# Performance work log

Hardware: AMD Instinct MI355X
Metric: run time of the kernel (lower is better)

Reference implementation:

```python
import jax, jax.numpy as jnp
import numpy as np


def _icosa_group():
    """60 rotation matrices of the icosahedral rotation group (vertex anchors)."""
    phi = (1.0 + 5.0 ** 0.5) / 2.0

    def rot(axis, ang):
        a = np.asarray(axis, dtype=np.float64)
        a = a / np.linalg.norm(a)
        K = np.array([[0.0, -a[2], a[1]], [a[2], 0.0, -a[0]], [-a[1], a[0], 0.0]])
        return np.eye(3) + np.sin(ang) * K + (1.0 - np.cos(ang)) * (K @ K)

    # two distinct 5-fold vertex axes generate the full group of order 60
    gens = [rot([0.0, 1.0, phi], 2.0 * np.pi / 5.0),
            rot([0.0, -1.0, phi], 2.0 * np.pi / 5.0)]
    mats = {tuple(np.round(np.eye(3), 6).ravel()): np.eye(3)}
    frontier = [np.eye(3)]
    while frontier:
        new = []
        for m in frontier:
            for g in gens:
                p = g @ m
                k = tuple(np.round(p, 6).ravel())
                if k not in mats:
                    mats[k] = p
                    new.append(p)
        frontier = new
    Rs = np.stack([mats[k] for k in sorted(mats.keys())]).astype(np.float32)
    assert Rs.shape[0] == 60
    return Rs


def _normalize(x, axis=-1, eps=1e-12):
    n = jnp.linalg.norm(x, axis=axis, keepdims=True)
    return x / jnp.maximum(n, eps)


def setup_inputs() -> dict:
    key = jax.random.key(0)
    ks = jax.random.split(key, 6)
    bs, P, N = 2, 1024, 16
    d_in, d_out, K = 64, 32, 7
    neighbor_index = jax.random.randint(ks[0], (bs, P, N), 0, P, dtype=jnp.int32)
    vertices = jax.random.normal(ks[1], (bs, P, 3), dtype=jnp.float32)
    feature_map = jax.random.normal(ks[2], (bs, d_in, P, 3), dtype=jnp.float32)
    W = jax.random.normal(ks[3], (d_out, d_in, K, 3), dtype=jnp.float32) * (2.0 / (d_in * K * 3 + d_out * K * 3)) ** 0.5
    W_center = jax.random.normal(ks[4], (d_out, d_in), dtype=jnp.float32) * (2.0 / (d_in + d_out)) ** 0.5
    directions = jax.random.normal(ks[5], (d_out, K, 3), dtype=jnp.float32) * (2.0 / (d_out * 3 + K * 3)) ** 0.5
    Rs = jnp.asarray(_icosa_group())
    return {"neighbor_index": neighbor_index, "vertices": vertices,
            "feature_map": feature_map, "W": W, "W_center": W_center,
            "directions": directions, "Rs": Rs}


def reference(neighbor_index, vertices, feature_map, W, W_center, directions, Rs):
    bs, P, N = neighbor_index.shape
    d_out, d_in, K, _ = W.shape
    n_bin = 5
    interval = Rs.shape[0] // n_bin

    # neighbor direction unit vectors [b,p,n,3]
    nbrs = jax.vmap(lambda v_b, i_b: v_b[i_b])(vertices, neighbor_index)
    ndn = _normalize(nbrs - vertices[:, :, None, :])
    kd = _normalize(directions)  # [d,k,3]

    # ---- stage 1: rotation search (fully detached in the torch original) ----
    ndn_s = jax.lax.stop_gradient(ndn)
    kd_s = jax.lax.stop_gradient(kd)
    W_s = jax.lax.stop_gradient(W)
    fm_s = jax.lax.stop_gradient(feature_map)
    Rs_s = jax.lax.stop_gradient(Rs)

    r_vals, r_idxs = [], []
    for i in range(n_bin):
        Rsi = Rs_s[i * interval:(i + 1) * interval]  # [r,3,3]
        kd_ro = jnp.einsum('dkj,rij->dkir', kd_s, Rsi)          # [d,k,3,r]
        theta = jnp.einsum('dkjr,bpnj->bdkpnr', kd_ro, ndn_s)   # [b,d,k,p,n,r]
        W_ro = jnp.einsum('dckj,rij->dckir', W_s, Rsi)          # [d,c,k,3,r]
        fo = jnp.einsum('dckir,bcpi->bdkpr', W_ro, fm_s)        # [b,d,k,p,r]
        gathered = jax.vmap(lambda f_b, i_b: f_b[:, :, i_b, :])(fo, neighbor_index)  # [b,d,k,p,n,r]
        ka = gathered * theta
        ka = jnp.max(ka, axis=4)   # max over neighbors -> [b,d,k,p,r]
        ka = jnp.sum(ka, axis=2)   # sum over kernel pts -> [b,d,p,r]
        r_vals.append(jnp.max(ka, axis=-1))
        r_idxs.append(jnp.argmax(ka, axis=-1) + i * interval)
    r_vals = jnp.stack(r_vals, axis=-1)  # [b,d,p,5]
    r_idxs = jnp.stack(r_idxs, axis=-1)  # [b,d,p,5]
    best_bin = jnp.argmax(r_vals, axis=-1)  # [b,d,p]
    r_index = jnp.take_along_axis(r_idxs, best_bin[..., None], axis=-1)[..., 0]  # [b,d,p]
    match_R = Rs[r_index]  # [b,d,p,3,3]

    # ---- stage 2: apply best rotation (differentiable) ----
    kd_ro2 = jnp.einsum('dkj,bdpij->bdkpi', kd, match_R)               # [b,d,k,p,3]
    theta2 = jax.nn.relu(jnp.einsum('bdkpj,bpnj->bdkpn', kd_ro2, ndn))  # [b,d,k,p,n]
    fo2 = jnp.einsum('dckj,bdpij,bcpi->bdkp', W, match_R, feature_map)  # [b,d,k,p]
    gathered2 = jax.vmap(lambda f_b, i_b: f_b[:, :, i_b])(fo2, neighbor_index)  # [b,d,k,p,n]
    ka2 = gathered2 * theta2
    kaw2 = jnp.max(ka2, axis=4)  # [b,d,k,p]
    out = jnp.einsum('bdkp,bdkpi->bdpi', kaw2, kd_ro2)
    center = jnp.einsum('dc,bcpi->bdpi', W_center, feature_map)
    return out + center
```

## Files before the change

### kernel.cpp

```cpp
#include <hip/hip_runtime.h>
#include <math.h>

#define BS   2
#define PP   1024
#define NN   16
#define CIN  64
#define DOUT 32
#define KK   7
#define NR   60
#define NT2  30

#define OFF_NDN  0
#define OFF_KROT 98304
#define OFF_M    138624
#define OFF_PVAL 4332928
#define OFF_PIDX 6299008
#define OFF_FO2  6790528
#define OFF_RIDX 7314816

#define NEG_INF (-3.402823466e38f)

typedef float v2f __attribute__((ext_vector_type(2)));
typedef float v4f __attribute__((ext_vector_type(4)));

__device__ __forceinline__ float sload(const float* __restrict__ p, int idx) {
    return __int_as_float(__builtin_amdgcn_readfirstlane(__float_as_int(p[idx])));
}

__device__ __forceinline__ v2f pk_mul_sv(v2f s, v2f v) {
    v2f d; asm("v_pk_mul_f32 %0, %1, %2" : "=v"(d) : "s"(s), "v"(v)); return d;
}
__device__ __forceinline__ v2f pk_fma_svv(v2f s, v2f v, v2f c) {
    v2f d; asm("v_pk_fma_f32 %0, %1, %2, %3" : "=v"(d) : "s"(s), "v"(v), "v"(c)); return d;
}
__device__ __forceinline__ v2f pk_mul_vv(v2f a, v2f b) {
    v2f d; asm("v_pk_mul_f32 %0, %1, %2" : "=v"(d) : "v"(a), "v"(b)); return d;
}

__device__ __forceinline__ float quad_max(float x) {
    float y = __int_as_float(__builtin_amdgcn_mov_dpp(
        __float_as_int(x), 0xB1, 0xF, 0xF, true));
    x = fmaxf(x, y);
    float z = __int_as_float(__builtin_amdgcn_mov_dpp(
        __float_as_int(x), 0x4E, 0xF, 0xF, true));
    return fmaxf(x, z);
}

__global__ __launch_bounds__(256) void k_pre(const int* __restrict__ nbr,
                                             const float* __restrict__ vert,
                                             const float* __restrict__ dirs,
                                             const float* __restrict__ Rs,
                                             float* __restrict__ ws) {
    int tid = blockIdx.x * 256 + threadIdx.x;
    if (tid < BS * PP * NN) {
        int p = (tid >> 4) & (PP - 1);
        int b = tid >> 14;
        int q = nbr[tid];
        const float* vp = vert + ((b << 10) + p) * 3;
        const float* vq = vert + ((b << 10) + q) * 3;
        float dx = vq[0] - vp[0], dy = vq[1] - vp[1], dz = vq[2] - vp[2];
        float nrm = sqrtf(dx * dx + dy * dy + dz * dz);
        float den = fmaxf(nrm, 1e-12f);
        dx /= den; dy /= den; dz /= den;
        float* o = ws + OFF_NDN + tid * 3;
        o[0] = dx; o[1] = dy; o[2] = dz;
    }
    int t2 = tid - BS * PP * NN;
    if (t2 >= 0 && t2 < DOUT * NR * KK) {
        int k = t2 % KK;
        int r = (t2 / KK) % NR;
        int d = t2 / (KK * NR);
        const float* dk = dirs + (d * KK + k) * 3;
        float x = dk[0], y = dk[1], z = dk[2];
        float nrm = sqrtf(x * x + y * y + z * z);
        float den = fmaxf(nrm, 1e-12f);
        x /= den; y /= den; z /= den;
        const float* R = Rs + r * 9;
        float* o = ws + OFF_KROT + t2 * 3;
        o[0] = R[0] * x + R[1] * y + R[2] * z;
        o[1] = R[3] * x + R[4] * y + R[5] * z;
        o[2] = R[6] * x + R[7] * y + R[8] * z;
    }
}

__global__ __launch_bounds__(256, 2) void k_buildM(const float* __restrict__ fm,
                                                   const float* __restrict__ W,
                                                   float* __restrict__ Mout) {
    int d = blockIdx.y, b = blockIdx.z;
    int p = blockIdx.x * 256 + threadIdx.x;

    float M[64];
#pragma unroll
    for (int t = 0; t < 64; t++) M[t] = 0.f;

    const float* fbase = fm + (size_t)(b * CIN * PP + p) * 3;
    const float* wbase = W + (size_t)d * CIN * KK * 3;
    for (int c = 0; c < CIN; c++) {
        const float* f = fbase + c * PP * 3;
        float f0 = f[0], f1 = f[1], f2 = f[2];
        const float* wl = wbase + c * 21;
#pragma unroll
        for (int k = 0; k < KK; k++) {
#pragma unroll
            for (int j = 0; j < 3; j++) {
                float w = sload(wl, k * 3 + j);
                M[k * 9 + 0 + j] += w * f0;
                M[k * 9 + 3 + j] += w * f1;
                M[k * 9 + 6 + j] += w * f2;
            }
        }
    }
    float4* o = (float4*)(Mout + (size_t)(((b * DOUT + d) << 10) + p) * 64);
#pragma unroll
    for (int t = 0; t < 15; t++)
        o[t] = make_float4(M[4 * t], M[4 * t + 1], M[4 * t + 2], M[4 * t + 3]);
    o[15] = make_float4(M[60], M[61], M[62], 0.f);
}

__device__ __forceinline__ int fo_base(int p) {
    return (p << 2) ^ ((p >> 1) & 7);
}

__global__ __launch_bounds__(1024)
void k_score(const int* __restrict__ nbr,
             const float* __restrict__ Rs,
             const float* __restrict__ Mptr,
             const float* __restrict__ ndn,
             const float* __restrict__ krot,
             float* __restrict__ pval,
             unsigned char* __restrict__ pidx8) {
    __shared__ v4f fo4s[PP * 4];
    const int tile = blockIdx.x, d = blockIdx.y, b = blockIdx.z;
    const int bd = b * DOUT + d;
    const int rbase = tile * 2;
    const int tq = threadIdx.x >> 2;
    const int ns = threadIdx.x & 3;

    {
        const int p = threadIdx.x;
        float Rc0[9], Rc1[9];
#pragma unroll
        for (int j = 0; j < 9; j++) {
            Rc0[j] = sload(Rs, (rbase + 0) * 9 + j);
            Rc1[j] = sload(Rs, (rbase + 1) * 9 + j);
        }
        float fo0[KK], fo1[KK];
#pragma unroll
        for (int k = 0; k < KK; k++) { fo0[k] = 0.f; fo1[k] = 0.f; }

        const float4* m4 = (const float4*)(Mptr + (size_t)((bd << 10) + p) * 64);
#pragma unroll
        for (int t = 0; t < 16; t++) {
            float4 v = m4[t];
            float e[4] = {v.x, v.y, v.z, v.w};
#pragma unroll
            for (int ee = 0; ee < 4; ee++) {
                const int g = 4 * t + ee;
                if (g < 63) {
                    const int k = g / 9, r9 = g % 9;
                    fo0[k] += Rc0[r9] * e[ee];
                    fo1[k] += Rc1[r9] * e[ee];
                }
            }
            if ((t & 3) == 3)
                __builtin_amdgcn_sched_barrier(0);
        }
        const int fb = fo_base(p);
        v4f s0; s0.x = fo0[0]; s0.y = fo1[0]; s0.z = fo0[1]; s0.w = fo1[1];
        v4f s1; s1.x = fo0[2]; s1.y = fo1[2]; s1.z = fo0[3]; s1.w = fo1[3];
        v4f s2; s2.x = fo0[4]; s2.y = fo1[4]; s2.z = fo0[5]; s2.w = fo1[5];
        v4f s3; s3.x = fo0[6]; s3.y = fo1[6]; s3.z = 0.f;    s3.w = 0.f;
        fo4s[fb]     = s0;
        fo4s[fb ^ 1] = s1;
        fo4s[fb ^ 2] = s2;
        fo4s[fb ^ 3] = s3;
    }
    __syncthreads();

    v2f vkp[KK][3];
    {
        const int kb0 = (d * NR + rbase + 0) * 21;
        const int kb1 = (d * NR + rbase + 1) * 21;
#pragma unroll
        for (int k = 0; k < KK; k++)
#pragma unroll
            for (int c = 0; c < 3; c++) {
                v2f t; t.x = sload(krot, kb0 + k * 3 + c);
                       t.y = sload(krot, kb1 + k * 3 + c);
                vkp[k][c] = t;
            }
    }
    const v2f* fo2s = (const v2f*)fo4s;

#pragma unroll
    for (int pp = 0; pp < 4; pp++) {
        const int p2 = (pp << 8) + tq;

        int4 nv = *(const int4*)(nbr + (((size_t)((b << 10) + p2)) << 4) + (ns << 2));
        float u[12];
        {
            const float4* u4 = (const float4*)(ndn + ((size_t)((b << 10) + p2) * 16 + (ns << 2)) * 3);
            float4 a = u4[0], bb = u4[1], cc = u4[2];
            u[0] = a.x;  u[1] = a.y;  u[2] = a.z;  u[3] = a.w;
            u[4] = bb.x; u[5] = bb.y; u[6] = bb.z; u[7] = bb.w;
            u[8] = cc.x; u[9] = cc.y; u[10] = cc.z; u[11] = cc.w;
        }

        float mk0[KK], mk1[KK];
#pragma unroll
        for (int k = 0; k < KK; k++) { mk0[k] = NEG_INF; mk1[k] = NEG_INF; }

        int c0 = fo_base(nv.x);
        v4f A = fo4s[c0];
        v4f B = fo4s[c0 ^ 1];
        v4f C = fo4s[c0 ^ 2];
        v2f D = fo2s[(c0 ^ 3) << 1];

#pragma unroll
        for (int n = 0; n < 4; n++) {
            v4f An, Bn, Cn; v2f Dn;
            if (n < 3) {
                int qn = (n == 0) ? nv.y : (n == 1) ? nv.z : nv.w;
                int cn = fo_base(qn);
                An = fo4s[cn];
                Bn = fo4s[cn ^ 1];
                Cn = fo4s[cn ^ 2];
                Dn = fo2s[(cn ^ 3) << 1];
            }
            float u0 = u[n * 3], u1 = u[n * 3 + 1], u2 = u[n * 3 + 2];
            v2f u00; u00.x = u0; u00.y = u0;
            v2f u11; u11.x = u1; u11.y = u1;
            v2f u22; u22.x = u2; u22.y = u2;
#pragma unroll
            for (int k = 0; k < KK; k++) {
                v2f g;
                if (k == 0)      g = __builtin_shufflevector(A, A, 0, 1);
                else if (k == 1) g = __builtin_shufflevector(A, A, 2, 3);
                else if (k == 2) g = __builtin_shufflevector(B, B, 0, 1);
                else if (k == 3) g = __builtin_shufflevector(B, B, 2, 3);
                else if (k == 4) g = __builtin_shufflevector(C, C, 0, 1);
                else if (k == 5) g = __builtin_shufflevector(C, C, 2, 3);
                else             g = D;
                v2f t = pk_mul_sv(vkp[k][0], u00);
                t = pk_fma_svv(vkp[k][1], u11, t);
                t = pk_fma_svv(vkp[k][2], u22, t);
                v2f pr = pk_mul_vv(g, t);
                mk0[k] = fmaxf(mk0[k], pr.x);
                mk1[k] = fmaxf(mk1[k], pr.y);
            }
            if (n < 3) { A = An; B = Bn; C = Cn; D = Dn; }
            __builtin_amdgcn_sched_barrier(0);
        }
#pragma unroll
        for (int k = 0; k < KK; k++) {
            mk0[k] = quad_max(mk0[k]);
            mk1[k] = quad_max(mk1[k]);
        }
        float s0 = ((mk0[0] + mk0[1]) + (mk0[2] + mk0[3])) + ((mk0[4] + mk0[5]) + mk0[6]);
        float s1 = ((mk1[0] + mk1[1]) + (mk1[2] + mk1[3])) + ((mk1[4] + mk1[5]) + mk1[6]);
        float bl = s0; int bil = rbase;
        if (s1 > bl) { bl = s1; bil = rbase + 1; }

        if (ns == 0) {
            int pi = (bd * NT2 + tile) * PP + p2;
            pval[pi] = bl;
            pidx8[pi] = (unsigned char)bil;
        }
    }
}

__global__ __launch_bounds__(256, 2) void k_reduce(const float* __restrict__ Rs,
                                                   float* __restrict__ ws) {
    int gid = blockIdx.x * 256 + threadIdx.x;
    int bd = gid >> 10;
    int p = gid & (PP - 1);
    const unsigned char* pidx8 = (const unsigned char*)(ws + OFF_PIDX);
    float best = NEG_INF;
    int bi = 0;
    for (int t = 0; t < NT2; t++) {
        float v = ws[OFF_PVAL + (bd * NT2 + t) * PP + p];
        int idx = pidx8[(bd * NT2 + t) * PP + p];
        if (v > best) { best = v; bi = idx; }
    }
    ((int*)ws)[OFF_RIDX + gid] = bi;

    const float* R = Rs + bi * 9;
    float R0 = R[0], R1 = R[1], R2 = R[2];
    float R3 = R[3], R4 = R[4], R5 = R[5];
    float R6 = R[6], R7 = R[7], R8 = R[8];

    float M[64];
    const float4* m4 = (const float4*)(ws + OFF_M + (size_t)gid * 64);
#pragma unroll
    for (int t = 0; t < 16; t++) {
        float4 v = m4[t];
        M[4 * t] = v.x; M[4 * t + 1] = v.y; M[4 * t + 2] = v.z; M[4 * t + 3] = v.w;
    }
    float* o = ws + OFF_FO2 + (size_t)gid * 8;
#pragma unroll
    for (int k = 0; k < KK; k++) {
        o[k] = R0 * M[k * 9 + 0] + R1 * M[k * 9 + 1] + R2 * M[k * 9 + 2]
             + R3 * M[k * 9 + 3] + R4 * M[k * 9 + 4] + R5 * M[k * 9 + 5]
             + R6 * M[k * 9 + 6] + R7 * M[k * 9 + 7] + R8 * M[k * 9 + 8];
    }
    o[7] = 0.f;
}

__global__ __launch_bounds__(256, 2) void k_final(const int* __restrict__ nbr,
                                                  const float* __restrict__ fm,
                                                  const float* __restrict__ Wc,
                                                  const float* __restrict__ ws,
                                                  float* __restrict__ out) {
    __shared__ float fo2_s[PP * 8];
    __shared__ float krot_s[NR * KK * 3];
    int d = blockIdx.y, b = blockIdx.z;
    int bd = b * DOUT + d;
    for (int i = threadIdx.x; i < PP * 8; i += 256)
        fo2_s[i] = ws[OFF_FO2 + (size_t)bd * PP * 8 + i];
    for (int i = threadIdx.x; i < NR * KK * 3; i += 256)
        krot_s[i] = ws[OFF_KROT + d * NR * KK * 3 + i];
    __syncthreads();

    int p = blockIdx.x * 256 + threadIdx.x;
    int gid = (bd << 10) + p;
    int ri = ((const int*)ws)[OFF_RIDX + gid];

    float v[21];
#pragma unroll
    for (int t = 0; t < 21; t++) v[t] = krot_s[ri * 21 + t];

    float u[48];
    {
        const float4* u4 = (const float4*)(ws + OFF_NDN + (size_t)((b << 10) + p) * 48);
#pragma unroll
        for (int t = 0; t < 12; t++) {
            float4 w = u4[t];
            u[4 * t] = w.x; u[4 * t + 1] = w.y; u[4 * t + 2] = w.z; u[4 * t + 3] = w.w;
        }
    }
    int nidx[16];
    {
        const int4* n4 = (const int4*)(nbr + (size_t)((b << 10) + p) * 16);
#pragma unroll
        for (int t = 0; t < 4; t++) {
            int4 w = n4[t];
            nidx[4 * t] = w.x; nidx[4 * t + 1] = w.y; nidx[4 * t + 2] = w.z; nidx[4 * t + 3] = w.w;
        }
    }

    float kaw[7];
#pragma unroll
    for (int k = 0; k < KK; k++) kaw[k] = NEG_INF;
#pragma unroll
    for (int n = 0; n < NN; n++) {
        int q = nidx[n];
        const float4* fq = (const float4*)&fo2_s[q * 8];
        float4 a = fq[0], c4 = fq[1];
        float g[7] = {a.x, a.y, a.z, a.w, c4.x, c4.y, c4.z};
        float u0 = u[n * 3], u1 = u[n * 3 + 1], u2 = u[n * 3 + 2];
#pragma unroll
        for (int k = 0; k < KK; k++) {
            float th = fmaxf(v[k * 3] * u0 + v[k * 3 + 1] * u1 + v[k * 3 + 2] * u2, 0.f);
            kaw[k] = fmaxf(kaw[k], g[k] * th);
        }
    }
    float o0 = 0.f, o1 = 0.f, o2 = 0.f;
#pragma unroll
    for (int k = 0; k < KK; k++) {
        o0 += kaw[k] * v[k * 3];
        o1 += kaw[k] * v[k * 3 + 1];
        o2 += kaw[k] * v[k * 3 + 2];
    }
    const float* fbase = fm + (size_t)(b * CIN * PP + p) * 3;
    const float* wrow = Wc + d * CIN;
    for (int c = 0; c < CIN; c++) {
        float wcv = sload(wrow, c);
        const float* f = fbase + c * PP * 3;
        o0 += wcv * f[0];
        o1 += wcv * f[1];
        o2 += wcv * f[2];
    }
    out[(size_t)gid * 3 + 0] = o0;
    out[(size_t)gid * 3 + 1] = o1;
    out[(size_t)gid * 3 + 2] = o2;
}

extern "C" void kernel_launch(void* const* d_in, const int* in_sizes, int n_in,
                              void* d_out, int out_size, void* d_ws, size_t ws_size,
                              hipStream_t stream) {
    const int*   nbr  = (const int*)d_in[0];
    const float* vert = (const float*)d_in[1];
    const float* fm   = (const float*)d_in[2];
    const float* W    = (const float*)d_in[3];
    const float* Wc   = (const float*)d_in[4];
    const float* dirs = (const float*)d_in[5];
    const float* Rs   = (const float*)d_in[6];
    float* ws  = (float*)d_ws;
    float* out = (float*)d_out;

    k_pre<<<181, 256, 0, stream>>>(nbr, vert, dirs, Rs, ws);
    k_buildM<<<dim3(PP / 256, DOUT, BS), 256, 0, stream>>>(fm, W, ws + OFF_M);
    k_score<<<dim3(NT2, DOUT, BS), 1024, 0, stream>>>(
        nbr, Rs, ws + OFF_M, ws + OFF_NDN, ws + OFF_KROT,
        ws + OFF_PVAL, (unsigned char*)(ws + OFF_PIDX));
    k_reduce<<<dim3(BS * DOUT * PP / 256), 256, 0, stream>>>(Rs, ws);
    k_final<<<dim3(PP / 256, DOUT, BS), 256, 0, stream>>>(nbr, fm, Wc, ws, out);
}
```

Baseline: 163.4 us.

## Fuse rotation reduce into final kernel and move center term into buildM

Removes the separate reduce kernel: each final block now reduces the per-tile best rotation, computes rotated fo2 for all points into shared memory, then runs the neighbor max with 4 threads per point and a quad max. The center-term matvec is computed once in buildM and stored to workspace. This drops a launch and the fo2/ridx global round trip, but each of the 4 blocks per (b,d) recomputes the full reduction and reads all of M, which adds redundant work.

Result: slower. 167.1 us (+2.2%).

```diff
diff --git a/kernel.cpp b/kernel.cpp
--- a/kernel.cpp
+++ b/kernel.cpp
@@ -15,8 +15,7 @@
 #define OFF_M    138624
 #define OFF_PVAL 4332928
 #define OFF_PIDX 6299008
-#define OFF_FO2  6790528
-#define OFF_RIDX 7314816
+#define OFF_CEN  6790528
 
 #define NEG_INF (-3.402823466e38f)
 
@@ -85,16 +84,20 @@
 
 __global__ __launch_bounds__(256, 2) void k_buildM(const float* __restrict__ fm,
                                                    const float* __restrict__ W,
-                                                   float* __restrict__ Mout) {
+                                                   const float* __restrict__ Wc,
+                                                   float* __restrict__ Mout,
+                                                   float* __restrict__ cen) {
     int d = blockIdx.y, b = blockIdx.z;
     int p = blockIdx.x * 256 + threadIdx.x;
 
     float M[64];
 #pragma unroll
     for (int t = 0; t < 64; t++) M[t] = 0.f;
+    float c0 = 0.f, c1 = 0.f, c2 = 0.f;
 
     const float* fbase = fm + (size_t)(b * CIN * PP + p) * 3;
     const float* wbase = W + (size_t)d * CIN * KK * 3;
+    const float* wrow = Wc + d * CIN;
     for (int c = 0; c < CIN; c++) {
         const float* f = fbase + c * PP * 3;
         float f0 = f[0], f1 = f[1], f2 = f[2];
@@ -109,16 +112,24 @@
                 M[k * 9 + 6 + j] += w * f2;
             }
         }
-    }
-    float4* o = (float4*)(Mout + (size_t)(((b * DOUT + d) << 10) + p) * 64);
+        float wcv = sload(wrow, c);
+        c0 += wcv * f0; c1 += wcv * f1; c2 += wcv * f2;
+    }
+    int gid = ((b * DOUT + d) << 10) + p;
+    float4* o = (float4*)(Mout + (size_t)gid * 64);
 #pragma unroll
     for (int t = 0; t < 15; t++)
         o[t] = make_float4(M[4 * t], M[4 * t + 1], M[4 * t + 2], M[4 * t + 3]);
     o[15] = make_float4(M[60], M[61], M[62], 0.f);
+    float* cp = cen + (size_t)gid * 3;
+    cp[0] = c0; cp[1] = c1; cp[2] = c2;
 }
 
 __device__ __forceinline__ int fo_base(int p) {
     return (p << 2) ^ ((p >> 1) & 7);
+}
+__device__ __forceinline__ int fo_s0(int p) {
+    return (p << 1) ^ ((p >> 2) & 7);
 }
 
 __global__ __launch_bounds__(1024)
@@ -269,120 +280,129 @@
     }
 }
 
-__global__ __launch_bounds__(256, 2) void k_reduce(const float* __restrict__ Rs,
-                                                   float* __restrict__ ws) {
-    int gid = blockIdx.x * 256 + threadIdx.x;
-    int bd = gid >> 10;
-    int p = gid & (PP - 1);
-    const unsigned char* pidx8 = (const unsigned char*)(ws + OFF_PIDX);
-    float best = NEG_INF;
-    int bi = 0;
-    for (int t = 0; t < NT2; t++) {
-        float v = ws[OFF_PVAL + (bd * NT2 + t) * PP + p];
-        int idx = pidx8[(bd * NT2 + t) * PP + p];
-        if (v > best) { best = v; bi = idx; }
-    }
-    ((int*)ws)[OFF_RIDX + gid] = bi;
-
-    const float* R = Rs + bi * 9;
-    float R0 = R[0], R1 = R[1], R2 = R[2];
-    float R3 = R[3], R4 = R[4], R5 = R[5];
-    float R6 = R[6], R7 = R[7], R8 = R[8];
-
-    float M[64];
-    const float4* m4 = (const float4*)(ws + OFF_M + (size_t)gid * 64);
-#pragma unroll
-    for (int t = 0; t < 16; t++) {
-        float4 v = m4[t];
-        M[4 * t] = v.x; M[4 * t + 1] = v.y; M[4 * t + 2] = v.z; M[4 * t + 3] = v.w;
-    }
-    float* o = ws + OFF_FO2 + (size_t)gid * 8;
-#pragma unroll
-    for (int k = 0; k < KK; k++) {
-        o[k] = R0 * M[k * 9 + 0] + R1 * M[k * 9 + 1] + R2 * M[k * 9 + 2]
-             + R3 * M[k * 9 + 3] + R4 * M[k * 9 + 4] + R5 * M[k * 9 + 5]
-             + R6 * M[k * 9 + 6] + R7 * M[k * 9 + 7] + R8 * M[k * 9 + 8];
-    }
-    o[7] = 0.f;
-}
-
-__global__ __launch_bounds__(256, 2) void k_final(const int* __restrict__ nbr,
-                                                  const float* __restrict__ fm,
-                                                  const float* __restrict__ Wc,
-                                                  const float* __restrict__ ws,
-                                                  float* __restrict__ out) {
-    __shared__ float fo2_s[PP * 8];
+__global__ __launch_bounds__(1024)
+void k_fin2(const int* __restrict__ nbr,
+            const float* __restrict__ Rs,
+            const float* __restrict__ Mptr,
+            const float* __restrict__ ndn,
+            const float* __restrict__ krot,
+            const float* __restrict__ pval,
+            const unsigned char* __restrict__ pidx8,
+            const float* __restrict__ cen,
+            float* __restrict__ out) {
+    __shared__ v4f fo4s[2 * PP];
+    __shared__ int ri_s[PP];
     __shared__ float krot_s[NR * KK * 3];
-    int d = blockIdx.y, b = blockIdx.z;
-    int bd = b * DOUT + d;
-    for (int i = threadIdx.x; i < PP * 8; i += 256)
-        fo2_s[i] = ws[OFF_FO2 + (size_t)bd * PP * 8 + i];
-    for (int i = threadIdx.x; i < NR * KK * 3; i += 256)
-        krot_s[i] = ws[OFF_KROT + d * NR * KK * 3 + i];
+    const int d = blockIdx.y, b = blockIdx.z;
+    const int bd = b * DOUT + d;
+
+    for (int i = threadIdx.x; i < NR * KK * 3; i += 1024)
+        krot_s[i] = krot[d * NR * KK * 3 + i];
+
+    {
+        const int p = threadIdx.x;
+        float best = NEG_INF;
+        int bi = 0;
+        for (int t = 0; t < NT2; t++) {
+            float v = pval[(bd * NT2 + t) * PP + p];
+            int idx = pidx8[(bd * NT2 + t) * PP + p];
+            if (v > best) { best = v; bi = idx; }
+        }
+        ri_s[p] = bi;
+
+        const float* R = Rs + bi * 9;
+        float R0 = R[0], R1 = R[1], R2 = R[2];
+        float R3 = R[3], R4 = R[4], R5 = R[5];
+        float R6 = R[6], R7 = R[7], R8 = R[8];
+
+        float fo[KK];
+#pragma unroll
+        for (int k = 0; k < KK; k++) fo[k] = 0.f;
+        const float4* m4 = (const float4*)(Mptr + (size_t)((bd << 10) + p) * 64);
+#pragma unroll
+        for (int t = 0; t < 16; t++) {
+            float4 v = m4[t];
+            float e[4] = {v.x, v.y, v.z, v.w};
+#pragma unroll
+            for (int ee = 0; ee < 4; ee++) {
+                const int g = 4 * t + ee;
+                if (g < 63) {
+                    const int k = g / 9, r9 = g % 9;
+                    float Rc = (r9 == 0) ? R0 : (r9 == 1) ? R1 : (r9 == 2) ? R2
+                             : (r9 == 3) ? R3 : (r9 == 4) ? R4 : (r9 == 5) ? R5
+                             : (r9 == 6) ? R6 : (r9 == 7) ? R7 : R8;
+                    fo[k] += Rc * e[ee];
+                }
+            }
+            if ((t & 3) == 3)
+                __builtin_amdgcn_sched_barrier(0);
+        }
+        const int s0 = fo_s0(p);
+        v4f a; a.x = fo[0]; a.y = fo[1]; a.z = fo[2]; a.w = fo[3];
+        v4f c; c.x = fo[4]; c.y = fo[5]; c.z = fo[6]; c.w = 0.f;
+        fo4s[s0]     = a;
+        fo4s[s0 ^ 1] = c;
+    }
     __syncthreads();
 
-    int p = blockIdx.x * 256 + threadIdx.x;
-    int gid = (bd << 10) + p;
-    int ri = ((const int*)ws)[OFF_RIDX + gid];
+    const int tq = threadIdx.x >> 2;
+    const int ns = threadIdx.x & 3;
+    const int p2 = (blockIdx.x << 8) + tq;
+    const int gid = (bd << 10) + p2;
+    const int ri = ri_s[p2];
 
     float v[21];
 #pragma unroll
     for (int t = 0; t < 21; t++) v[t] = krot_s[ri * 21 + t];
 
-    float u[48];
+    int nidx[4];
     {
-        const float4* u4 = (const float4*)(ws + OFF_NDN + (size_t)((b << 10) + p) * 48);
-#pragma unroll
-        for (int t = 0; t < 12; t++) {
-            float4 w = u4[t];
-            u[4 * t] = w.x; u[4 * t + 1] = w.y; u[4 * t + 2] = w.z; u[4 * t + 3] = w.w;
-        }
-    }
-    int nidx[16];
+        int4 w = *(const int4*)(nbr + (((size_t)((b << 10) + p2)) << 4) + (ns << 2));
+        nidx[0] = w.x; nidx[1] = w.y; nidx[2] = w.z; nidx[3] = w.w;
+    }
+    float u[12];
     {
-        const int4* n4 = (const int4*)(nbr + (size_t)((b << 10) + p) * 16);
-#pragma unroll
-        for (int t = 0; t < 4; t++) {
-            int4 w = n4[t];
-            nidx[4 * t] = w.x; nidx[4 * t + 1] = w.y; nidx[4 * t + 2] = w.z; nidx[4 * t + 3] = w.w;
-        }
-    }
-
-    float kaw[7];
+        const float4* u4 = (const float4*)(ndn + ((size_t)((b << 10) + p2) * 16 + (ns << 2)) * 3);
+        float4 a = u4[0], bb = u4[1], cc = u4[2];
+        u[0] = a.x;  u[1] = a.y;  u[2] = a.z;  u[3] = a.w;
+        u[4] = bb.x; u[5] = bb.y; u[6] = bb.z; u[7] = bb.w;
+        u[8] = cc.x; u[9] = cc.y; u[10] = cc.z; u[11] = cc.w;
+    }
+
+    float kaw[KK];
 #pragma unroll
     for (int k = 0; k < KK; k++) kaw[k] = NEG_INF;
 #pragma unroll
-    for (int n = 0; n < NN; n++) {
+    for (int n = 0; n < 4; n++) {
         int q = nidx[n];
-        const float4* fq = (const float4*)&fo2_s[q * 8];
-        float4 a = fq[0], c4 = fq[1];
-        float g[7] = {a.x, a.y, a.z, a.w, c4.x, c4.y, c4.z};
+        int s = fo_s0(q);
+        v4f A = fo4s[s];
+        v4f Bv = fo4s[s ^ 1];
+        float g[7] = {A.x, A.y, A.z, A.w, Bv.x, Bv.y, Bv.z};
         float u0 = u[n * 3], u1 = u[n * 3 + 1], u2 = u[n * 3 + 2];
 #pragma unroll
         for (int k = 0; k < KK; k++) {
             float th = fmaxf(v[k * 3] * u0 + v[k * 3 + 1] * u1 + v[k * 3 + 2] * u2, 0.f);
             kaw[k] = fmaxf(kaw[k], g[k] * th);
         }
-    }
-    float o0 = 0.f, o1 = 0.f, o2 = 0.f;
-#pragma unroll
-    for (int k = 0; k < KK; k++) {
-        o0 += kaw[k] * v[k * 3];
-        o1 += kaw[k] * v[k * 3 + 1];
-        o2 += kaw[k] * v[k * 3 + 2];
-    }
-    const float* fbase = fm + (size_t)(b * CIN * PP + p) * 3;
-    const float* wrow = Wc + d * CIN;
-    for (int c = 0; c < CIN; c++) {
-        float wcv = sload(wrow, c);
-        const float* f = fbase + c * PP * 3;
-        o0 += wcv * f[0];
-        o1 += wcv * f[1];
-        o2 += wcv * f[2];
-    }
-    out[(size_t)gid * 3 + 0] = o0;
-    out[(size_t)gid * 3 + 1] = o1;
-    out[(size_t)gid * 3 + 2] = o2;
+        __builtin_amdgcn_sched_barrier(0);
+    }
+#pragma unroll
+    for (int k = 0; k < KK; k++) kaw[k] = quad_max(kaw[k]);
+
+    if (ns == 0) {
+        float o0 = 0.f, o1 = 0.f, o2 = 0.f;
+#pragma unroll
+        for (int k = 0; k < KK; k++) {
+            o0 += kaw[k] * v[k * 3];
+            o1 += kaw[k] * v[k * 3 + 1];
+            o2 += kaw[k] * v[k * 3 + 2];
+        }
+        const float* cp = cen + (size_t)gid * 3;
+        out[(size_t)gid * 3 + 0] = o0 + cp[0];
+        out[(size_t)gid * 3 + 1] = o1 + cp[1];
+        out[(size_t)gid * 3 + 2] = o2 + cp[2];
+    }
 }
 
 extern "C" void kernel_launch(void* const* d_in, const int* in_sizes, int n_in,
@@ -399,10 +419,13 @@
     float* out = (float*)d_out;
 
     k_pre<<<181, 256, 0, stream>>>(nbr, vert, dirs, Rs, ws);
-    k_buildM<<<dim3(PP / 256, DOUT, BS), 256, 0, stream>>>(fm, W, ws + OFF_M);
+    k_buildM<<<dim3(PP / 256, DOUT, BS), 256, 0, stream>>>(
+        fm, W, Wc, ws + OFF_M, ws + OFF_CEN);
     k_score<<<dim3(NT2, DOUT, BS), 1024, 0, stream>>>(
         nbr, Rs, ws + OFF_M, ws + OFF_NDN, ws + OFF_KROT,
         ws + OFF_PVAL, (unsigned char*)(ws + OFF_PIDX));
-    k_reduce<<<dim3(BS * DOUT * PP / 256), 256, 0, stream>>>(Rs, ws);
-    k_final<<<dim3(PP / 256, DOUT, BS), 256, 0, stream>>>(nbr, fm, Wc, ws, out);
-}
+    k_fin2<<<dim3(PP / 256, DOUT, BS), 1024, 0, stream>>>(
+        nbr, Rs, ws + OFF_M, ws + OFF_NDN, ws + OFF_KROT,
+        ws + OFF_PVAL, (const unsigned char*)(ws + OFF_PIDX),
+        ws + OFF_CEN, out);
+}
```
